# Kernel tuning notes

Hardware: AMD Instinct MI355X
Metric: run time of the kernel (lower is better)

The kernel has to match this reference:

```python
import jax, jax.numpy as jnp
import numpy as np

D_MODEL = 1024
N_HEADS = 16
D_HEAD = 64
BATCH = 4
SEQ = 2048
NEG = -1000000000.0


def setup_inputs() -> dict:
    key = jax.random.key(0)
    k1, k2, k3, k4, k5 = jax.random.split(key, 5)
    x = jax.random.normal(k1, (BATCH, SEQ, D_MODEL), dtype=jnp.float32)
    std = 0.02
    wq = jax.random.normal(k2, (N_HEADS, D_HEAD, D_MODEL), dtype=jnp.float32) * std
    wk = jax.random.normal(k3, (N_HEADS, D_HEAD, D_MODEL), dtype=jnp.float32) * std
    wv = jax.random.normal(k4, (N_HEADS, D_HEAD, D_MODEL), dtype=jnp.float32) * std
    wo = jax.random.normal(k5, (D_MODEL, N_HEADS * D_HEAD), dtype=jnp.float32) * std
    return {"x": x, "wq": wq, "wk": wk, "wv": wv, "wo": wo}


def reference(x, wq, wk, wv, wo):
    # x: [b, s, d_model]; wq/wk/wv: [h, d_head, d_model]; wo: [d_model, h*d_head]
    b, s, _ = x.shape
    scale = jnp.sqrt(jnp.asarray(D_HEAD, x.dtype))
    q = jnp.einsum('bsd,hed->bhse', x, wq)
    k = jnp.einsum('bsd,hed->bhse', x, wk)
    v = jnp.einsum('bsd,hed->bhse', x, wv)
    scores = jnp.einsum('bhse,bhte->bhst', q, k) / scale
    causal_mask = jnp.triu(jnp.ones((s, s), dtype=bool), k=1)
    scores = jnp.where(causal_mask, jnp.asarray(NEG, scores.dtype), scores)
    weights = jax.nn.softmax(scores, axis=-1)
    heads = jnp.einsum('bhst,bhte->bhse', weights, v)  # [b, h, s, d_head]
    concat = heads.transpose(0, 2, 1, 3).reshape(b, s, N_HEADS * D_HEAD)
    return concat @ wo.T
```

## Files before the change

kernel.cpp:

```cpp
#include <hip/hip_runtime.h>


#define DEV __device__ __forceinline__

typedef __attribute__((ext_vector_type(8))) __bf16 bf16x8;
typedef __attribute__((ext_vector_type(4))) float f32x4;
typedef unsigned short u16;

struct alignas(8) U16x4 { u16 x, y, z, w; };

DEV u16 f2bf(float f) {
  unsigned int u = __builtin_bit_cast(unsigned int, f);
  u = u + 0x7FFFu + ((u >> 16) & 1u);
  return (u16)(u >> 16);
}

DEV unsigned cvt_pk_bf16(float a, float b) {
  unsigned r;
  asm("v_cvt_pk_bf16_f32 %0, %1, %2" : "=v"(r) : "v"(a), "v"(b));
  return r;
}

DEV f32x4 mfma16(uint2 a, uint2 b, f32x4 c) {
  f32x4 d;
  asm("v_mfma_f32_16x16x16_bf16 %0, %1, %2, %3" : "=v"(d) : "v"(a), "v"(b), "v"(c));
  return d;
}

DEV void gload_lds16(const void* g, void* l) {
  __builtin_amdgcn_global_load_lds(
      (const __attribute__((address_space(1))) unsigned int*)g,
      (__attribute__((address_space(3))) unsigned int*)l, 16, 0, 0);
}

__global__ void cast_kernel(const float* __restrict__ in, u16* __restrict__ out, int n4) {
  int i = blockIdx.x * blockDim.x + threadIdx.x;
  if (i >= n4) return;
  const float4 v = reinterpret_cast<const float4*>(in)[i];
  U16x4 o{f2bf(v.x), f2bf(v.y), f2bf(v.z), f2bf(v.w)};
  reinterpret_cast<U16x4*>(out)[i] = o;
}

__global__ void cast_w_kernel(const float* __restrict__ wq, const float* __restrict__ wk,
                              const float* __restrict__ wv, const float* __restrict__ wo,
                              u16* __restrict__ wqkvb, u16* __restrict__ wob) {
  const int y = blockIdx.y;
  const int i = blockIdx.x * blockDim.x + threadIdx.x;
  const float* src = (y == 0) ? wq : (y == 1) ? wk : (y == 2) ? wv : wo;
  u16* dst = (y < 3) ? (wqkvb + (size_t)y * 1048576) : wob;
  const float4 v = reinterpret_cast<const float4*>(src)[i];
  U16x4 o{f2bf(v.x), f2bf(v.y), f2bf(v.z), f2bf(v.w)};
  reinterpret_cast<U16x4*>(dst)[i] = o;
}

template <int MODE, int NBN>
__global__ __launch_bounds__(256) void gemm_bt(
    const u16* __restrict__ A, const u16* __restrict__ B,
    void* __restrict__ C0, u16* __restrict__ vtp, int N) {
  constexpr int K = 1024;
  const int d = blockIdx.x;
  const int chunk = gridDim.x >> 3;
  const int vg = (d & 7) * chunk + (d >> 3);
  const int bn = vg % NBN, bm = vg / NBN;
  const int tid = threadIdx.x;
  const int w = tid >> 6, lane = tid & 63, lo = lane & 15, hi = lane >> 4;
  const int wm = w >> 1, wn = w & 1;

  __shared__ char lds[65536];
  char* sA = lds;
  char* sB = lds + 32768;

  const u16* Ag = A + (size_t)(bm * 128) * K;
  const u16* Bg = B + (size_t)(bn * 128) * K;

  f32x4 acc[4][4] = {};

  auto stage = [&](int buf, int k0) {
#pragma unroll
    for (int it = 0; it < 4; ++it) {
      const int L = (it * 4 + w) * 64 + lane;
      const int r = L >> 3, p = L & 7, c = p ^ (r & 7);
      gload_lds16(Ag + (size_t)r * K + k0 + c * 8, sA + buf * 16384 + (it * 4 + w) * 1024);
      gload_lds16(Bg + (size_t)r * K + k0 + c * 8, sB + buf * 16384 + (it * 4 + w) * 1024);
    }
  };

  stage(0, 0);
  __syncthreads();
  int cur = 0;
  for (int t = 0; t < 16; ++t) {
    if (t + 1 < 16) stage(cur ^ 1, (t + 1) * 64);
#pragma unroll
    for (int kc = 0; kc < 2; ++kc) {
      bf16x8 af[4], bfr[4];
#pragma unroll
      for (int m = 0; m < 4; ++m) {
        const int r = wm * 64 + m * 16 + lo;
        const int p = (kc * 4 + hi) ^ (r & 7);
        af[m] = *reinterpret_cast<const bf16x8*>(sA + cur * 16384 + r * 128 + p * 16);
      }
#pragma unroll
      for (int n = 0; n < 4; ++n) {
        const int r = wn * 64 + n * 16 + lo;
        const int p = (kc * 4 + hi) ^ (r & 7);
        bfr[n] = *reinterpret_cast<const bf16x8*>(sB + cur * 16384 + r * 128 + p * 16);
      }
#pragma unroll
      for (int m = 0; m < 4; ++m)
#pragma unroll
        for (int n = 0; n < 4; ++n)
          acc[m][n] = __builtin_amdgcn_mfma_f32_16x16x32_bf16(af[m], bfr[n], acc[m][n], 0, 0, 0);
    }
    __syncthreads();
    cur ^= 1;
  }

  const int colW = bn * 128 + wn * 64;
  const int rowW = bm * 128 + wm * 64;
  if (MODE == 0) {
    float* C = (float*)C0;
#pragma unroll
    for (int m = 0; m < 4; ++m)
#pragma unroll
      for (int n = 0; n < 4; ++n) {
        const int col = colW + n * 16 + lo;
        const int rb = rowW + m * 16 + hi * 4;
#pragma unroll
        for (int rg = 0; rg < 4; ++rg)
          C[(size_t)(rb + rg) * N + col] = acc[m][n][rg];
      }
  } else {
    u16* qkvp = (u16*)C0;
    if (bn * 128 < 2048) {
      const float qs = (bn < 8) ? 0.18033688011112042f : 1.0f;
#pragma unroll
      for (int m = 0; m < 4; ++m)
#pragma unroll
        for (int n = 0; n < 4; ++n) {
          const int col = colW + n * 16 + lo;
          const int rb = rowW + m * 16 + hi * 4;
#pragma unroll
          for (int rg = 0; rg < 4; ++rg)
            qkvp[(size_t)(rb + rg) * 2048 + col] = f2bf(acc[m][n][rg] * qs);
        }
    } else {
#pragma unroll
      for (int m = 0; m < 4; ++m)
#pragma unroll
        for (int n = 0; n < 4; ++n) {
          const int col = colW + n * 16 + lo;
          const int idx = col - 2048;
          const int hh = idx >> 6, e = idx & 63;
          const int rb = rowW + m * 16 + hi * 4;
          const int bb = rb >> 11, s = rb & 2047;
          U16x4 v4{f2bf(acc[m][n][0]), f2bf(acc[m][n][1]),
                   f2bf(acc[m][n][2]), f2bf(acc[m][n][3])};
          *reinterpret_cast<U16x4*>(vtp + ((size_t)((bb * 16 + hh) * 64 + e)) * 2048 + s) = v4;
        }
    }
  }
}

__global__ __launch_bounds__(512, 4) void attn_kernel(
    const u16* __restrict__ qkv, const u16* __restrict__ vt, u16* __restrict__ heads) {
  const int dd = blockIdx.x;
  const int vg = (dd & 7) * 64 + (dd >> 3);
  const int bx = vg & 7, bh = vg >> 3;
  const int b = bh >> 4, h = bh & 15;
  const int tid = threadIdx.x;
  const int w = tid >> 6, lane = tid & 63, lo = lane & 15, hi = lane >> 4;

  __shared__ char lds[81920];
  char* sQP = lds;
  char* sK  = lds + 16384;
  char* sV  = lds + 49152;

  const u16* Kg = qkv + (size_t)(b * 2048) * 2048 + 1024 + h * 64;
  const u16* Vg = vt + (size_t)bh * 64 * 2048;

  const int kr = tid >> 3, kc_ = (tid & 7) ^ (kr & 7);
  const int vr = tid >> 4, vc_ = (tid & 15) ^ (vr & 7);
  auto stageKV = [&](int buf, int kv0) {
#pragma unroll
    for (int it = 0; it < 2; ++it) {
      gload_lds16(Kg + (size_t)(kv0 + it * 64 + kr) * 2048 + kc_ * 8,
                  sK + buf * 16384 + it * 8192 + w * 1024);
      gload_lds16(Vg + (size_t)(it * 32 + vr) * 2048 + kv0 + vc_ * 8,
                  sV + buf * 16384 + it * 8192 + w * 1024);
    }
  };

  const int qloc = w * 16 + lo;

  for (int rep = 0; rep < 2; ++rep) {
    const int qt = rep ? (15 - bx) : bx;
    const u16* Qg = qkv + (size_t)(b * 2048 + qt * 128) * 2048 + h * 64;

#pragma unroll
    for (int it = 0; it < 2; ++it)
      gload_lds16(Qg + (size_t)(it * 64 + kr) * 2048 + kc_ * 8, sQP + it * 8192 + w * 1024);
    stageKV(0, 0);
    __syncthreads();

    bf16x8 qf[2];
#pragma unroll
    for (int kc = 0; kc < 2; ++kc) {
      const int p = (kc * 4 + hi) ^ (lo & 7);
      qf[kc] = *reinterpret_cast<const bf16x8*>(sQP + qloc * 128 + p * 16);
    }

    f32x4 lvec = {};
    f32x4 oacc[4] = {};

    const int nt = qt + 1;

    auto step = [&](int t, int cur) {
      if (t + 1 < nt) stageKV(cur ^ 1, (t + 1) * 128);
      f32x4 sa[8] = {};
      __builtin_amdgcn_s_setprio(1);
#pragma unroll
      for (int kc = 0; kc < 2; ++kc) {
#pragma unroll
        for (int n = 0; n < 8; ++n) {
          const int r = n * 16 + lo;
          const int p = (kc * 4 + hi) ^ (lo & 7);
          const bf16x8 kf = *reinterpret_cast<const bf16x8*>(sK + cur * 16384 + r * 128 + p * 16);
          sa[n] = __builtin_amdgcn_mfma_f32_16x16x32_bf16(kf, qf[kc], sa[n], 0, 0, 0);
        }
      }
      __builtin_amdgcn_s_setprio(0);

      if (t == nt - 1) {
#pragma unroll
        for (int n = 0; n < 8; ++n)
#pragma unroll
          for (int rg = 0; rg < 4; ++rg)
            if (n * 16 + hi * 4 + rg > qloc) sa[n][rg] = -1e9f;
      }

#pragma unroll
      for (int n = 0; n < 8; ++n)
#pragma unroll
        for (int rg = 0; rg < 4; ++rg) sa[n][rg] = exp2f(sa[n][rg]);
      lvec += ((sa[0] + sa[1]) + (sa[2] + sa[3])) + ((sa[4] + sa[5]) + (sa[6] + sa[7]));

      __builtin_amdgcn_s_setprio(1);
#pragma unroll
      for (int n = 0; n < 8; ++n) {
        const uint2 pb{cvt_pk_bf16(sa[n][0], sa[n][1]), cvt_pk_bf16(sa[n][2], sa[n][3])};
        const int sb = (((2 * n + (hi >> 1)) ^ (lo & 7)) << 4) + ((hi & 1) << 3);
#pragma unroll
        for (int ne = 0; ne < 4; ++ne) {
          const uint2 vf = *reinterpret_cast<const uint2*>(
              sV + cur * 16384 + (ne * 16 + lo) * 256 + sb);
          oacc[ne] = mfma16(vf, pb, oacc[ne]);
        }
      }
      __builtin_amdgcn_s_setprio(0);
      __syncthreads();
    };

    for (int i = 0; i < nt; i += 2) {
      step(i, 0);
      if (i + 1 < nt) step(i + 1, 1);
    }

    float lsum = (lvec[0] + lvec[1]) + (lvec[2] + lvec[3]);
    lsum += __shfl_xor(lsum, 16);
    lsum += __shfl_xor(lsum, 32);
    const float inv = 1.0f / lsum;
    const int q = qt * 128 + qloc;
    u16* dst = heads + (size_t)(b * 2048 + q) * 1024 + h * 64;
#pragma unroll
    for (int ne = 0; ne < 4; ++ne) {
      const unsigned r0 = cvt_pk_bf16(oacc[ne][0] * inv, oacc[ne][1] * inv);
      const unsigned r1 = cvt_pk_bf16(oacc[ne][2] * inv, oacc[ne][3] * inv);
      *reinterpret_cast<uint2*>(dst + ne * 16 + hi * 4) = uint2{r0, r1};
    }
  }
}

extern "C" void kernel_launch(void* const* d_in, const int* in_sizes, int n_in,
                              void* d_out, int out_size, void* d_ws, size_t ws_size,
                              hipStream_t stream) {
  const float* x  = (const float*)d_in[0];
  const float* wq = (const float*)d_in[1];
  const float* wk = (const float*)d_in[2];
  const float* wv = (const float*)d_in[3];
  const float* wo = (const float*)d_in[4];

  char* ws = (char*)d_ws;
  u16* xb    = (u16*)(ws);
  u16* wqkvb = (u16*)(ws + 16777216);
  u16* wob   = (u16*)(ws + 23068672);
  u16* qkv   = (u16*)(ws + 25165824);
  u16* vtp   = (u16*)(ws + 58720256);
  u16* heads = (u16*)(ws + 75497472);

  cast_kernel<<<8192, 256, 0, stream>>>(x, xb, 2097152);
  cast_w_kernel<<<dim3(1024, 4), 256, 0, stream>>>(wq, wk, wv, wo, wqkvb, wob);

  gemm_bt<1, 24><<<1536, 256, 0, stream>>>(xb, wqkvb, qkv, vtp, 3072);
  attn_kernel<<<512, 512, 0, stream>>>(qkv, vtp, heads);
  gemm_bt<0, 8><<<512, 256, 0, stream>>>(heads, wob, d_out, nullptr, 1024);
}
```

Baseline: 178.3 us.

## Enlarge attention query tile to 256 rows with two query groups per wave

```diff
diff --git a/kernel.cpp b/kernel.cpp
--- a/kernel.cpp
+++ b/kernel.cpp
@@ -161,19 +161,19 @@
   }
 }
 
-__global__ __launch_bounds__(512, 4) void attn_kernel(
+__global__ __launch_bounds__(512, 2) void attn_kernel(
     const u16* __restrict__ qkv, const u16* __restrict__ vt, u16* __restrict__ heads) {
   const int dd = blockIdx.x;
-  const int vg = (dd & 7) * 64 + (dd >> 3);
-  const int bx = vg & 7, bh = vg >> 3;
+  const int vg = (dd & 7) * 32 + (dd >> 3);
+  const int bx = vg & 3, bh = vg >> 2;
   const int b = bh >> 4, h = bh & 15;
   const int tid = threadIdx.x;
   const int w = tid >> 6, lane = tid & 63, lo = lane & 15, hi = lane >> 4;
 
-  __shared__ char lds[81920];
+  __shared__ char lds[98304];
   char* sQP = lds;
-  char* sK  = lds + 16384;
-  char* sV  = lds + 49152;
+  char* sK  = lds + 32768;
+  char* sV  = lds + 65536;
 
   const u16* Kg = qkv + (size_t)(b * 2048) * 2048 + 1024 + h * 64;
   const u16* Vg = vt + (size_t)bh * 64 * 2048;
@@ -190,73 +190,94 @@
     }
   };
 
-  const int qloc = w * 16 + lo;
+  const int qw = w * 32;
 
   for (int rep = 0; rep < 2; ++rep) {
-    const int qt = rep ? (15 - bx) : bx;
-    const u16* Qg = qkv + (size_t)(b * 2048 + qt * 128) * 2048 + h * 64;
-
-#pragma unroll
-    for (int it = 0; it < 2; ++it)
-      gload_lds16(Qg + (size_t)(it * 64 + kr) * 2048 + kc_ * 8, sQP + it * 8192 + w * 1024);
+    const int qt = rep ? (7 - bx) : bx;
+    const u16* Qg = qkv + (size_t)(b * 2048 + qt * 256) * 2048 + h * 64;
+
+#pragma unroll
+    for (int it = 0; it < 4; ++it) {
+      const int L = it * 512 + tid;
+      const int r = L >> 3, c = (L & 7) ^ (kr & 7);
+      gload_lds16(Qg + (size_t)r * 2048 + c * 8, sQP + it * 8192 + w * 1024);
+    }
     stageKV(0, 0);
     __syncthreads();
 
-    bf16x8 qf[2];
-#pragma unroll
-    for (int kc = 0; kc < 2; ++kc) {
-      const int p = (kc * 4 + hi) ^ (lo & 7);
-      qf[kc] = *reinterpret_cast<const bf16x8*>(sQP + qloc * 128 + p * 16);
-    }
-
-    f32x4 lvec = {};
-    f32x4 oacc[4] = {};
-
-    const int nt = qt + 1;
+    bf16x8 qf[2][2];
+#pragma unroll
+    for (int qg = 0; qg < 2; ++qg)
+#pragma unroll
+      for (int kc = 0; kc < 2; ++kc) {
+        const int r = qw + qg * 16 + lo;
+        const int p = (kc * 4 + hi) ^ (lo & 7);
+        qf[qg][kc] = *reinterpret_cast<const bf16x8*>(sQP + r * 128 + p * 16);
+      }
+
+    f32x4 lvec[2] = {};
+    f32x4 oacc[2][4] = {};
+
+    const int nt = 2 * qt + 2;
+    const int qmaxw = qt * 256 + qw + 31;
 
     auto step = [&](int t, int cur) {
       if (t + 1 < nt) stageKV(cur ^ 1, (t + 1) * 128);
-      f32x4 sa[8] = {};
-      __builtin_amdgcn_s_setprio(1);
-#pragma unroll
-      for (int kc = 0; kc < 2; ++kc) {
+      if (t * 128 <= qmaxw) {
+        f32x4 sa[2][8] = {};
+        __builtin_amdgcn_s_setprio(1);
+#pragma unroll
+        for (int kc = 0; kc < 2; ++kc) {
+#pragma unroll
+          for (int n = 0; n < 8; ++n) {
+            const int r = n * 16 + lo;
+            const int p = (kc * 4 + hi) ^ (lo & 7);
+            const bf16x8 kf = *reinterpret_cast<const bf16x8*>(sK + cur * 16384 + r * 128 + p * 16);
+            sa[0][n] = __builtin_amdgcn_mfma_f32_16x16x32_bf16(kf, qf[0][kc], sa[0][n], 0, 0, 0);
+            sa[1][n] = __builtin_amdgcn_mfma_f32_16x16x32_bf16(kf, qf[1][kc], sa[1][n], 0, 0, 0);
+          }
+        }
+        __builtin_amdgcn_s_setprio(0);
+
+        if (t >= nt - 2) {
+          const int kb = t * 128 - qt * 256;
+#pragma unroll
+          for (int qg = 0; qg < 2; ++qg) {
+            const int ql = qw + qg * 16 + lo;
+#pragma unroll
+            for (int n = 0; n < 8; ++n)
+#pragma unroll
+              for (int rg = 0; rg < 4; ++rg)
+                if (kb + n * 16 + hi * 4 + rg > ql) sa[qg][n][rg] = -1e9f;
+          }
+        }
+
+#pragma unroll
+        for (int qg = 0; qg < 2; ++qg) {
+#pragma unroll
+          for (int n = 0; n < 8; ++n)
+#pragma unroll
+            for (int rg = 0; rg < 4; ++rg) sa[qg][n][rg] = exp2f(sa[qg][n][rg]);
+          lvec[qg] += ((sa[qg][0] + sa[qg][1]) + (sa[qg][2] + sa[qg][3])) +
+                      ((sa[qg][4] + sa[qg][5]) + (sa[qg][6] + sa[qg][7]));
+        }
+
+        __builtin_amdgcn_s_setprio(1);
 #pragma unroll
         for (int n = 0; n < 8; ++n) {
-          const int r = n * 16 + lo;
-          const int p = (kc * 4 + hi) ^ (lo & 7);
-          const bf16x8 kf = *reinterpret_cast<const bf16x8*>(sK + cur * 16384 + r * 128 + p * 16);
-          sa[n] = __builtin_amdgcn_mfma_f32_16x16x32_bf16(kf, qf[kc], sa[n], 0, 0, 0);
-        }
-      }
-      __builtin_amdgcn_s_setprio(0);
-
-      if (t == nt - 1) {
-#pragma unroll
-        for (int n = 0; n < 8; ++n)
-#pragma unroll
-          for (int rg = 0; rg < 4; ++rg)
-            if (n * 16 + hi * 4 + rg > qloc) sa[n][rg] = -1e9f;
-      }
-
-#pragma unroll
-      for (int n = 0; n < 8; ++n)
-#pragma unroll
-        for (int rg = 0; rg < 4; ++rg) sa[n][rg] = exp2f(sa[n][rg]);
-      lvec += ((sa[0] + sa[1]) + (sa[2] + sa[3])) + ((sa[4] + sa[5]) + (sa[6] + sa[7]));
-
-      __builtin_amdgcn_s_setprio(1);
-#pragma unroll
-      for (int n = 0; n < 8; ++n) {
-        const uint2 pb{cvt_pk_bf16(sa[n][0], sa[n][1]), cvt_pk_bf16(sa[n][2], sa[n][3])};
-        const int sb = (((2 * n + (hi >> 1)) ^ (lo & 7)) << 4) + ((hi & 1) << 3);
-#pragma unroll
-        for (int ne = 0; ne < 4; ++ne) {
-          const uint2 vf = *reinterpret_cast<const uint2*>(
-              sV + cur * 16384 + (ne * 16 + lo) * 256 + sb);
-          oacc[ne] = mfma16(vf, pb, oacc[ne]);
-        }
-      }
-      __builtin_amdgcn_s_setprio(0);
+          const uint2 pb0{cvt_pk_bf16(sa[0][n][0], sa[0][n][1]), cvt_pk_bf16(sa[0][n][2], sa[0][n][3])};
+          const uint2 pb1{cvt_pk_bf16(sa[1][n][0], sa[1][n][1]), cvt_pk_bf16(sa[1][n][2], sa[1][n][3])};
+          const int sb = (((2 * n + (hi >> 1)) ^ (lo & 7)) << 4) + ((hi & 1) << 3);
+#pragma unroll
+          for (int ne = 0; ne < 4; ++ne) {
+            const uint2 vf = *reinterpret_cast<const uint2*>(
+                sV + cur * 16384 + (ne * 16 + lo) * 256 + sb);
+            oacc[0][ne] = mfma16(vf, pb0, oacc[0][ne]);
+            oacc[1][ne] = mfma16(vf, pb1, oacc[1][ne]);
+          }
+        }
+        __builtin_amdgcn_s_setprio(0);
+      }
       __syncthreads();
     };
 
@@ -265,17 +286,20 @@
       if (i + 1 < nt) step(i + 1, 1);
     }
 
-    float lsum = (lvec[0] + lvec[1]) + (lvec[2] + lvec[3]);
-    lsum += __shfl_xor(lsum, 16);
-    lsum += __shfl_xor(lsum, 32);
-    const float inv = 1.0f / lsum;
-    const int q = qt * 128 + qloc;
-    u16* dst = heads + (size_t)(b * 2048 + q) * 1024 + h * 64;
-#pragma unroll
-    for (int ne = 0; ne < 4; ++ne) {
-      const unsigned r0 = cvt_pk_bf16(oacc[ne][0] * inv, oacc[ne][1] * inv);
-      const unsigned r1 = cvt_pk_bf16(oacc[ne][2] * inv, oacc[ne][3] * inv);
-      *reinterpret_cast<uint2*>(dst + ne * 16 + hi * 4) = uint2{r0, r1};
+#pragma unroll
+    for (int qg = 0; qg < 2; ++qg) {
+      float lsum = (lvec[qg][0] + lvec[qg][1]) + (lvec[qg][2] + lvec[qg][3]);
+      lsum += __shfl_xor(lsum, 16);
+      lsum += __shfl_xor(lsum, 32);
+      const float inv = 1.0f / lsum;
+      const int q = qt * 256 + qw + qg * 16 + lo;
+      u16* dst = heads + (size_t)(b * 2048 + q) * 1024 + h * 64;
+#pragma unroll
+      for (int ne = 0; ne < 4; ++ne) {
+        const unsigned r0 = cvt_pk_bf16(oacc[qg][ne][0] * inv, oacc[qg][ne][1] * inv);
+        const unsigned r1 = cvt_pk_bf16(oacc[qg][ne][2] * inv, oacc[qg][ne][3] * inv);
+        *reinterpret_cast<uint2*>(dst + ne * 16 + hi * 4) = uint2{r0, r1};
+      }
     }
   }
 }
@@ -301,6 +325,6 @@
   cast_w_kernel<<<dim3(1024, 4), 256, 0, stream>>>(wq, wk, wv, wo, wqkvb, wob);
 
   gemm_bt<1, 24><<<1536, 256, 0, stream>>>(xb, wqkvb, qkv, vtp, 3072);
-  attn_kernel<<<512, 512, 0, stream>>>(qkv, vtp, heads);
+  attn_kernel<<<256, 512, 0, stream>>>(qkv, vtp, heads);
   gemm_bt<0, 8><<<512, 256, 0, stream>>>(heads, wob, d_out, nullptr, 1024);
 }
```

Result: no change. 179.4 us (+0.6%).
